# Kernel optimization log

Hardware: AMD Instinct MI355X
Metric: run time of the kernel (lower is better)

Reference implementation:

```python
import jax, jax.numpy as jnp
import numpy as np
import math

T, B, C, F, H, LF, GF = 1024, 8, 512, 64, 8, 64, 64


def setup_inputs() -> dict:
    key = jax.random.key(0)
    ks = jax.random.split(key, 24)
    s = 0.02  # weight init scale for stability through the recurrence
    rn = lambda k, shp, sc=1.0: jax.random.normal(k, shp, jnp.float32) * sc
    inp = {
        "x": rn(ks[0], (B, T, C)),
        "ln_g": jnp.ones((C,), jnp.float32),
        "ln_b": jnp.zeros((C,), jnp.float32),
        "tl_initial": rn(ks[1], (C,)),
        "tl_premix": jax.random.uniform(ks[2], (C,), jnp.float32),
        "tl_w1": rn(ks[3], (C, LF), s), "tl_b1": jnp.zeros((LF,), jnp.float32),
        "tl_w2": rn(ks[4], (LF, C), s), "tl_b2": jnp.zeros((C,), jnp.float32),
        "bias": jnp.zeros((C,), jnp.float32),
        "gating_res": jax.random.uniform(ks[5], (C,), jnp.float32),
        "g_w1": rn(ks[6], (C, GF), s), "g_b1": jnp.zeros((GF,), jnp.float32),
        "g_w2": rn(ks[7], (GF, C), s), "g_b2": jnp.zeros((C,), jnp.float32),
        "dn_initial": rn(ks[8], (H, F, F)),
        "A_w": rn(ks[9], (H, C, F), s), "A_b": rn(ks[10], (H, F), s),
        "B_w": jnp.zeros((H, C, F), jnp.float32), "B_b": rn(ks[11], (H, F), s),
        "C_w": rn(ks[12], (H, C, F), s), "C_b": rn(ks[13], (H, F), s),
        "D_w": rn(ks[14], (H, C, F), s), "D_b": rn(ks[15], (H, F), s),
        "I_w": rn(ks[16], (H, C, F), s), "I_b": rn(ks[17], (H, F), s),
        "S_w": rn(ks[18], (H, C, F), s), "S_b": rn(ks[19], (H, F), s),
        "O_w": rn(ks[20], (H, F, C), s),
    }
    return inp


def _deltanet_head(y, init_state, Aw, Ab, Bw, Bb, Cw, Cb, Dw, Db, Iw, Ib, Sw, Sb, Ow):
    # y: [T, B, C]; init_state: [F, F]
    f = init_state.shape[-1]
    sf = math.sqrt(f)  # awk_safe
    a = y @ Aw + Ab   # [T,B,F]
    b = y @ Bw + Bb
    c = y @ Cw + Cb
    d = y @ Dw + Db
    i = y @ Iw + Ib
    sel = y @ Sw + Sb
    st0 = jnp.broadcast_to(init_state, (y.shape[1], f, f)).astype(y.dtype)

    def step(st, ins):
        sel_t, a_t, b_t, c_t, d_t, i_t = ins  # each [B,F]
        st = (st * jax.nn.sigmoid(i_t)[:, None, :]
              + jnp.einsum('bij,bj->bi', st, a_t)[:, :, None] * b_t[:, None, :] / sf
              + c_t[:, :, None] * d_t[:, None, :])
        out = jnp.einsum('bf,bfg->bg', sel_t, st)
        return st, out

    st, o = jax.lax.scan(step, st0, (sel, a, b, c, d, i))
    return o @ Ow, st  # [T,B,C]


def reference(x, ln_g, ln_b, tl_initial, tl_premix, tl_w1, tl_b1, tl_w2, tl_b2,
              bias, gating_res, g_w1, g_b1, g_w2, g_b2, dn_initial,
              A_w, A_b, B_w, B_b, C_w, C_b, D_w, D_b, I_w, I_b, S_w, S_b, O_w):
    xt = jnp.swapaxes(x, 0, -2)  # [T, B, C] (time_dim=-2)
    res = xt
    # LayerNorm (eps=1e-5)
    mu = jnp.mean(xt, -1, keepdims=True)
    var = jnp.mean((xt - mu) ** 2, -1, keepdims=True)
    h = (xt - mu) / jnp.sqrt(var + 1e-5) * ln_g + ln_b
    # TokenLerp (state=None -> xf[0]=initial)
    xf = jnp.concatenate([jnp.broadcast_to(tl_initial, (1,) + h.shape[1:]).astype(h.dtype), h[:-1]], axis=0)
    pm = h + (xf - h) * tl_premix
    decide = jax.nn.sigmoid(jax.nn.gelu(pm @ tl_w1 + tl_b1, approximate=False) @ tl_w2 + tl_b2)
    h = h + (xf - h) * decide
    # y starts from bias; heads are chained sequentially (y feeds next head)
    y = jnp.broadcast_to(bias, h.shape).astype(h.dtype)
    for k in range(dn_initial.shape[0]):
        y, _ = _deltanet_head(y, dn_initial[k], A_w[k], A_b[k], B_w[k], B_b[k],
                              C_w[k], C_b[k], D_w[k], D_b[k], I_w[k], I_b[k],
                              S_w[k], S_b[k], O_w[k])
    gate = jax.nn.sigmoid(jax.nn.gelu((y + h * gating_res) @ g_w1 + g_b1, approximate=False) @ g_w2 + g_b2)
    # use_residual=True path: returns res + y (no transpose back, matching source)
    return res + y * gate
```

## Files before the change

### kernel.cpp

```cpp
#include <hip/hip_runtime.h>
#include <hip/hip_bf16.h>

#define T_DIM 1024
#define B_DIM 8
#define C_DIM 512
#define F_DIM 64
#define H_DIM 8
#define CHUNK 32
#define NCHUNK 32

__device__ __forceinline__ float sigmoidf_(float v) { return 1.0f / (1.0f + __expf(-v)); }
__device__ __forceinline__ float geluf_(float v) { return 0.5f * v * (1.0f + erff(v * 0.70710678118654752f)); }
__device__ __forceinline__ float rl_(float v, int l) {
  return __uint_as_float(__builtin_amdgcn_readlane(__float_as_uint(v), l));
}

struct GemmArgs {
  const float* A; const float* W; const float* bias; float* out;
  int M, K, N;
  const float* x; const float* mu; const float* rstd;
  const float* ln_g; const float* ln_b; const float* tl_initial; const float* premix;
  const float* yv; const float* gres;
  float* h2;
  const float* Wg[6]; const float* bg[6];
};

struct AFetch {
  float4 v0, v1, v2, v3, v4;
  float s0, s1, s2, s3;
};

template<int MODE_A>
__device__ __forceinline__ AFetch a_fetch(const GemmArgs& g, int r, int c) {
  AFetch f; f.s0 = f.s1 = f.s2 = f.s3 = 0.f;
  if (MODE_A == 0) {
    f.v0 = *(const float4*)&g.A[r * g.K + c];
  } else if (MODE_A == 1) {
    const int b = r & 7, t = r >> 3;
    f.v0 = *(const float4*)&g.x[(b * T_DIM + t) * C_DIM + c];
    f.s0 = g.mu[r]; f.s1 = g.rstd[r];
    if (t > 0) {
      f.v1 = *(const float4*)&g.x[(b * T_DIM + t - 1) * C_DIM + c];
      f.s2 = g.mu[r - 8]; f.s3 = g.rstd[r - 8];
    } else {
      f.v1 = *(const float4*)&g.tl_initial[c];
    }
    f.v2 = *(const float4*)&g.ln_g[c];
    f.v3 = *(const float4*)&g.ln_b[c];
    f.v4 = *(const float4*)&g.premix[c];
  } else {
    f.v0 = *(const float4*)&g.yv[(r >> 3) * C_DIM + c];
    f.v1 = *(const float4*)&g.h2[r * C_DIM + c];
    f.v2 = *(const float4*)&g.gres[c];
  }
  return f;
}

template<int MODE_A>
__device__ __forceinline__ float4 a_combine(const AFetch& f, int r) {
  if (MODE_A == 0) return f.v0;
  float4 o;
  float* op = (float*)&o;
  const float* xa = (const float*)&f.v0;
  const float* xb = (const float*)&f.v1;
  const float* lg = (const float*)&f.v2;
  const float* lb = (const float*)&f.v3;
  const float* pm = (const float*)&f.v4;
  if (MODE_A == 1) {
    const int t = r >> 3;
    #pragma unroll
    for (int q = 0; q < 4; ++q) {
      float h  = (xa[q] - f.s0) * f.s1 * lg[q] + lb[q];
      float xf = (t == 0) ? xb[q] : (xb[q] - f.s2) * f.s3 * lg[q] + lb[q];
      op[q] = h + (xf - h) * pm[q];
    }
    return o;
  }
  #pragma unroll
  for (int q = 0; q < 4; ++q)
    op[q] = xa[q] + xb[q] * lg[q];
  return o;
}

template<int MODE_B>
__device__ __forceinline__ float4 w_fetch(const GemmArgs& g, int kk, int n0, int tc) {
  if (MODE_B == 1)
    return *(const float4*)&g.Wg[blockIdx.y][kk * 64 + (tc << 2)];
  return *(const float4*)&g.W[kk * g.N + n0 + (tc << 2)];
}

template<int MODE_A, int MODE_B, int EPI>
__global__ __launch_bounds__(256) void gemm_kernel(GemmArgs g) {
  __shared__ float AsT[16][68];
  __shared__ float Bs[16][64];
  const int m0 = blockIdx.x * 64, n0 = blockIdx.y * 64;
  const int tid = threadIdx.x;
  const int tr = tid >> 4, tc = tid & 15;
  const int ai = tid >> 2, aj = (tid & 3) << 2;
  const float scg = (MODE_B == 1 && blockIdx.y == 1) ? 0.125f : 1.0f;
  float acc[4][4] = {};
  AFetch fa = a_fetch<MODE_A>(g, m0 + ai, aj);
  float4 wv = w_fetch<MODE_B>(g, tr, n0, tc);
  for (int k0 = 0; k0 < g.K; k0 += 16) {
    if (k0) __syncthreads();
    const float4 av = a_combine<MODE_A>(fa, m0 + ai);
    AsT[aj + 0][ai] = av.x;
    AsT[aj + 1][ai] = av.y;
    AsT[aj + 2][ai] = av.z;
    AsT[aj + 3][ai] = av.w;
    *(float4*)&Bs[tr][tc << 2] =
        make_float4(wv.x * scg, wv.y * scg, wv.z * scg, wv.w * scg);
    if (k0 + 16 < g.K) {
      fa = a_fetch<MODE_A>(g, m0 + ai, k0 + 16 + aj);
      wv = w_fetch<MODE_B>(g, k0 + 16 + tr, n0, tc);
    }
    __syncthreads();
    #pragma unroll
    for (int kk = 0; kk < 16; ++kk) {
      const float4 a4 = *(const float4*)&AsT[kk][tr << 2];
      const float4 b4 = *(const float4*)&Bs[kk][tc << 2];
      const float avr[4] = {a4.x, a4.y, a4.z, a4.w};
      const float bvr[4] = {b4.x, b4.y, b4.z, b4.w};
      #pragma unroll
      for (int r_ = 0; r_ < 4; ++r_)
        #pragma unroll
        for (int c_ = 0; c_ < 4; ++c_)
          acc[r_][c_] = fmaf(avr[r_], bvr[c_], acc[r_][c_]);
    }
  }
  #pragma unroll
  for (int r_ = 0; r_ < 4; ++r_) {
    const int rr = m0 + (tr << 2) + r_;
    #pragma unroll
    for (int c_ = 0; c_ < 4; ++c_) {
      const int lc = (tc << 2) + c_;
      const int cc = n0 + lc;
      float v = acc[r_][c_];
      if (MODE_B == 1) v += g.bg[blockIdx.y][lc] * scg;
      else if (g.bias) v += g.bias[cc];
      if (EPI == 0) {
        g.out[rr * g.N + cc] = v;
      } else if (EPI == 1) {
        g.out[rr * g.N + cc] = geluf_(v);
      } else if (EPI == 2) {
        float d = sigmoidf_(v);
        const int b = rr & 7, t = rr >> 3;
        float xv = g.x[(b * T_DIM + t) * C_DIM + cc];
        float h = (xv - g.mu[rr]) * g.rstd[rr] * g.ln_g[cc] + g.ln_b[cc];
        float xf;
        if (t == 0) xf = g.tl_initial[cc];
        else {
          float xp = g.x[(b * T_DIM + t - 1) * C_DIM + cc];
          xf = (xp - g.mu[rr - 8]) * g.rstd[rr - 8] * g.ln_g[cc] + g.ln_b[cc];
        }
        g.h2[rr * C_DIM + cc] = h + (xf - h) * d;
      } else {
        float gate = sigmoidf_(v);
        const int b = rr & 7, t = rr >> 3;
        float res = g.x[(b * T_DIM + t) * C_DIM + cc];
        g.out[rr * C_DIM + cc] = res + g.yv[t * C_DIM + cc] * gate;
      }
    }
  }
}

__global__ __launch_bounds__(256) void ln_stats_kernel(const float* __restrict__ x,
                                                       float* __restrict__ mu,
                                                       float* __restrict__ rstd,
                                                       const float* __restrict__ bias,
                                                       float* __restrict__ y) {
  const int gid = blockIdx.x * 256 + threadIdx.x;
  y[gid] = bias[gid & (C_DIM - 1)];
  const int row = blockIdx.x * 4 + (threadIdx.x >> 6);
  const int lane = threadIdx.x & 63;
  const int b = row & 7, t = row >> 3;
  const float* xr = x + (b * T_DIM + t) * C_DIM;
  float4 v0 = *(const float4*)&xr[lane * 8];
  float4 v1 = *(const float4*)&xr[lane * 8 + 4];
  float s  = v0.x + v0.y + v0.z + v0.w + v1.x + v1.y + v1.z + v1.w;
  float s2 = v0.x*v0.x + v0.y*v0.y + v0.z*v0.z + v0.w*v0.w
           + v1.x*v1.x + v1.y*v1.y + v1.z*v1.z + v1.w*v1.w;
  #pragma unroll
  for (int m = 1; m < 64; m <<= 1) { s += __shfl_xor(s, m); s2 += __shfl_xor(s2, m); }
  if (lane == 0) {
    float mean = s * (1.0f / 512.0f);
    float var = s2 * (1.0f / 512.0f) - mean * mean;
    mu[row] = mean;
    rstd[row] = rsqrtf(var + 1e-5f);
  }
}


__global__ __launch_bounds__(256) void scan_phaseA(const float* __restrict__ PRJ,
                                                   float* __restrict__ chPT,
                                                   float* __restrict__ chS) {
  const int j = blockIdx.x;
  const int tid = threadIdx.x;
  const int ri = tid >> 4, ci = tid & 15;
  float Pm[4][4], Sm[4][4];
  #pragma unroll
  for (int r = 0; r < 4; ++r)
    #pragma unroll
    for (int c = 0; c < 4; ++c) {
      Pm[r][c] = (ri * 4 + r == ci * 4 + c) ? 1.0f : 0.0f;
      Sm[r][c] = 0.0f;
    }
  const float* base = PRJ + j * CHUNK * 384;
  float4 pa = *(const float4*)&base[      ci * 4];
  float4 pb = *(const float4*)&base[ 64 + ci * 4];
  float4 pc = *(const float4*)&base[128 + ri * 4];
  float4 pd = *(const float4*)&base[192 + ci * 4];
  float4 pi = *(const float4*)&base[256 + ci * 4];
  for (int s = 0; s < CHUNK; ++s) {
    float4 na = pa, nb = pb, nc2 = pc, nd = pd, ni = pi;
    if (s + 1 < CHUNK) {
      const float* b2 = base + (s + 1) * 384;
      na  = *(const float4*)&b2[      ci * 4];
      nb  = *(const float4*)&b2[ 64 + ci * 4];
      nc2 = *(const float4*)&b2[128 + ri * 4];
      nd  = *(const float4*)&b2[192 + ci * 4];
      ni  = *(const float4*)&b2[256 + ci * 4];
    }
    const float sg[4] = {sigmoidf_(pi.x), sigmoidf_(pi.y), sigmoidf_(pi.z), sigmoidf_(pi.w)};
    const float aa[4] = {pa.x, pa.y, pa.z, pa.w};
    const float bb2[4] = {pb.x, pb.y, pb.z, pb.w};
    const float cv[4] = {pc.x, pc.y, pc.z, pc.w};
    const float dd[4] = {pd.x, pd.y, pd.z, pd.w};
    float rp[4], rs[4];
    #pragma unroll
    for (int r = 0; r < 4; ++r) {
      rp[r] = Pm[r][0]*aa[0] + Pm[r][1]*aa[1] + Pm[r][2]*aa[2] + Pm[r][3]*aa[3];
      rs[r] = Sm[r][0]*aa[0] + Sm[r][1]*aa[1] + Sm[r][2]*aa[2] + Sm[r][3]*aa[3];
    }
    #pragma unroll
    for (int m = 1; m <= 8; m <<= 1) {
      #pragma unroll
      for (int r = 0; r < 4; ++r) {
        rp[r] += __shfl_xor(rp[r], m);
        rs[r] += __shfl_xor(rs[r], m);
      }
    }
    #pragma unroll
    for (int r = 0; r < 4; ++r)
      #pragma unroll
      for (int c = 0; c < 4; ++c) {
        Pm[r][c] = Pm[r][c] * sg[c] + rp[r] * bb2[c];
        Sm[r][c] = Sm[r][c] * sg[c] + rs[r] * bb2[c] + cv[r] * dd[c];
      }
    pa = na; pb = nb; pc = nc2; pd = nd; pi = ni;
  }
  float* cpT = chPT + j * 4096;
  float* cs  = chS + j * 4096;
  #pragma unroll
  for (int c = 0; c < 4; ++c)
    *(float4*)&cpT[(ci*4+c)*64 + ri*4] =
        make_float4(Pm[0][c], Pm[1][c], Pm[2][c], Pm[3][c]);
  #pragma unroll
  for (int r = 0; r < 4; ++r)
    *(float4*)&cs[(ri*4+r)*64 + ci*4] = make_float4(Sm[r][0], Sm[r][1], Sm[r][2], Sm[r][3]);
}

__device__ __forceinline__ float cstep(const float4 (&P)[16], float sv, float rv) {
  float p0 = 0.f, p1 = 0.f, p2 = 0.f, p3 = 0.f;
  #pragma unroll
  for (int q = 0; q < 16; ++q) {
    p0 = fmaf(rl_(rv, q * 4 + 0), P[q].x, p0);
    p1 = fmaf(rl_(rv, q * 4 + 1), P[q].y, p1);
    p2 = fmaf(rl_(rv, q * 4 + 2), P[q].z, p2);
    p3 = fmaf(rl_(rv, q * 4 + 3), P[q].w, p3);
  }
  return sv + ((p0 + p1) + (p2 + p3));
}

__global__ __launch_bounds__(64) void scan_combine(const float* __restrict__ st0,
                                                   const float* __restrict__ chPT,
                                                   const float* __restrict__ chS,
                                                   float* __restrict__ bnd) {
  const int lane = threadIdx.x;
  const int r = blockIdx.x;
  float rv = st0[r * 64 + lane];
  const float* basePT = chPT + lane * 64;
  const float* baseS  = chS + r * 64 + lane;
  float* bndRL = bnd + r * 64 + lane;
  for (int j = 0; j < NCHUNK; ++j) {
    float4 P[16];
    const float* pp = basePT + j * 4096;
    #pragma unroll
    for (int q = 0; q < 16; ++q) P[q] = *(const float4*)&pp[q * 4];
    const float sv = baseS[j * 4096];
    bndRL[j * 4096] = rv;
    rv = cstep(P, sv, rv);
  }
}

__global__ __launch_bounds__(256) void scan_phaseC(const float* __restrict__ PRJ,
                                                   const float* __restrict__ bnd,
                                                   const float* __restrict__ Ow,
                                                   float* __restrict__ y) {
  __shared__ float olds[CHUNK][4][64];
  __shared__ float osT[64][CHUNK + 1];
  const int j = blockIdx.x;
  const int tid = threadIdx.x;
  const int ri = tid >> 4, ci = tid & 15, w = tid >> 6;
  float st[4][4];
  #pragma unroll
  for (int r = 0; r < 4; ++r) {
    const float4 v = *(const float4*)&bnd[j*4096 + (ri*4+r)*64 + ci*4];
    st[r][0] = v.x; st[r][1] = v.y; st[r][2] = v.z; st[r][3] = v.w;
  }
  const float* base = PRJ + j * CHUNK * 384;
  float4 pa = *(const float4*)&base[      ci * 4];
  float4 pb = *(const float4*)&base[ 64 + ci * 4];
  float4 pc = *(const float4*)&base[128 + ri * 4];
  float4 pd = *(const float4*)&base[192 + ci * 4];
  float4 pi = *(const float4*)&base[256 + ci * 4];
  float4 ps = *(const float4*)&base[320 + ri * 4];
  for (int s = 0; s < CHUNK; ++s) {
    float4 na = pa, nb = pb, nc2 = pc, nd = pd, ni = pi, ns = ps;
    if (s + 1 < CHUNK) {
      const float* b2 = base + (s + 1) * 384;
      na  = *(const float4*)&b2[      ci * 4];
      nb  = *(const float4*)&b2[ 64 + ci * 4];
      nc2 = *(const float4*)&b2[128 + ri * 4];
      nd  = *(const float4*)&b2[192 + ci * 4];
      ni  = *(const float4*)&b2[256 + ci * 4];
      ns  = *(const float4*)&b2[320 + ri * 4];
    }
    const float sg[4] = {sigmoidf_(pi.x), sigmoidf_(pi.y), sigmoidf_(pi.z), sigmoidf_(pi.w)};
    const float aa[4] = {pa.x, pa.y, pa.z, pa.w};
    const float bb2[4] = {pb.x, pb.y, pb.z, pb.w};
    const float cv[4] = {pc.x, pc.y, pc.z, pc.w};
    const float dd[4] = {pd.x, pd.y, pd.z, pd.w};
    const float ss[4] = {ps.x, ps.y, ps.z, ps.w};
    float rd[4];
    #pragma unroll
    for (int r = 0; r < 4; ++r)
      rd[r] = st[r][0]*aa[0] + st[r][1]*aa[1] + st[r][2]*aa[2] + st[r][3]*aa[3];
    #pragma unroll
    for (int m = 1; m <= 8; m <<= 1) {
      #pragma unroll
      for (int r = 0; r < 4; ++r) rd[r] += __shfl_xor(rd[r], m);
    }
    float po[4] = {0.f, 0.f, 0.f, 0.f};
    #pragma unroll
    for (int r = 0; r < 4; ++r)
      #pragma unroll
      for (int c = 0; c < 4; ++c) {
        const float nv = st[r][c] * sg[c] + rd[r] * bb2[c] + cv[r] * dd[c];
        st[r][c] = nv;
        po[c] = fmaf(ss[r], nv, po[c]);
      }
    #pragma unroll
    for (int c = 0; c < 4; ++c) {
      po[c] += __shfl_xor(po[c], 16);
      po[c] += __shfl_xor(po[c], 32);
    }
    if ((tid & 48) == 0)
      *(float4*)&olds[s][w][ci * 4] = make_float4(po[0], po[1], po[2], po[3]);
    pa = na; pb = nb; pc = nc2; pd = nd; pi = ni; ps = ns;
  }
  __syncthreads();
  #pragma unroll
  for (int e = 0; e < 8; ++e) {
    const int id = tid + 256 * e;
    const int f = id & 63, t = id >> 6;
    osT[f][t] = olds[t][0][f] + olds[t][1][f] + olds[t][2][f] + olds[t][3][f];
  }
  __syncthreads();
  const int c0 = tid << 1;
  float2 acc[CHUNK];
  #pragma unroll
  for (int t = 0; t < CHUNK; ++t) acc[t] = make_float2(0.f, 0.f);
  #pragma unroll 1
  for (int fo = 0; fo < 8; ++fo) {
    float2 ow[8];
    #pragma unroll
    for (int q = 0; q < 8; ++q)
      ow[q] = *(const float2*)&Ow[(fo * 8 + q) * C_DIM + c0];
    #pragma unroll
    for (int q = 0; q < 8; ++q) {
      const int f = fo * 8 + q;
      #pragma unroll
      for (int t8 = 0; t8 < 8; ++t8) {
        const float4 ov = *(const float4*)&osT[f][t8 * 4];
        acc[t8*4+0].x = fmaf(ov.x, ow[q].x, acc[t8*4+0].x);
        acc[t8*4+0].y = fmaf(ov.x, ow[q].y, acc[t8*4+0].y);
        acc[t8*4+1].x = fmaf(ov.y, ow[q].x, acc[t8*4+1].x);
        acc[t8*4+1].y = fmaf(ov.y, ow[q].y, acc[t8*4+1].y);
        acc[t8*4+2].x = fmaf(ov.z, ow[q].x, acc[t8*4+2].x);
        acc[t8*4+2].y = fmaf(ov.z, ow[q].y, acc[t8*4+2].y);
        acc[t8*4+3].x = fmaf(ov.w, ow[q].x, acc[t8*4+3].x);
        acc[t8*4+3].y = fmaf(ov.w, ow[q].y, acc[t8*4+3].y);
      }
    }
  }
  #pragma unroll
  for (int t = 0; t < CHUNK; ++t)
    *(float2*)&y[(j * CHUNK + t) * C_DIM + c0] = acc[t];
}

extern "C" void kernel_launch(void* const* d_in, const int* in_sizes, int n_in,
                              void* d_out, int out_size, void* d_ws, size_t ws_size,
                              hipStream_t stream) {
  const float* x       = (const float*)d_in[0];
  const float* ln_g    = (const float*)d_in[1];
  const float* ln_b    = (const float*)d_in[2];
  const float* tl_init = (const float*)d_in[3];
  const float* premix  = (const float*)d_in[4];
  const float* tl_w1   = (const float*)d_in[5];
  const float* tl_b1   = (const float*)d_in[6];
  const float* tl_w2   = (const float*)d_in[7];
  const float* tl_b2   = (const float*)d_in[8];
  const float* bias    = (const float*)d_in[9];
  const float* gres    = (const float*)d_in[10];
  const float* g_w1    = (const float*)d_in[11];
  const float* g_b1    = (const float*)d_in[12];
  const float* g_w2    = (const float*)d_in[13];
  const float* g_b2    = (const float*)d_in[14];
  const float* dn_init = (const float*)d_in[15];
  const float* A_w     = (const float*)d_in[16];
  const float* A_b     = (const float*)d_in[17];
  const float* B_w     = (const float*)d_in[18];
  const float* B_b     = (const float*)d_in[19];
  const float* C_w     = (const float*)d_in[20];
  const float* C_b     = (const float*)d_in[21];
  const float* D_w     = (const float*)d_in[22];
  const float* D_b     = (const float*)d_in[23];
  const float* I_w     = (const float*)d_in[24];
  const float* I_b     = (const float*)d_in[25];
  const float* S_w     = (const float*)d_in[26];
  const float* S_b     = (const float*)d_in[27];
  const float* O_w     = (const float*)d_in[28];

  float* ws      = (float*)d_ws;
  float* mu      = ws;
  float* rstd    = mu + 8192;
  float* hidden1 = rstd + 8192;
  float* y       = hidden1 + 524288;
  float* PRJ     = y + 524288;
  float* chPT    = PRJ + 393216;
  float* chS     = chPT + 131072;
  float* bnd     = chS + 131072;
  float* h2      = (float*)d_out;

  ln_stats_kernel<<<2048, 256, 0, stream>>>(x, mu, rstd, bias, y);

  GemmArgs ga = {};
  ga.x = x; ga.mu = mu; ga.rstd = rstd; ga.ln_g = ln_g; ga.ln_b = ln_b;
  ga.tl_initial = tl_init; ga.premix = premix; ga.gres = gres; ga.h2 = h2;

  {
    GemmArgs g = ga; g.W = tl_w1; g.bias = tl_b1; g.out = hidden1;
    g.M = 8192; g.K = 512; g.N = 64;
    gemm_kernel<1, 0, 1><<<dim3(128, 1), 256, 0, stream>>>(g);
  }
  {
    GemmArgs g = ga; g.A = hidden1; g.W = tl_w2; g.bias = tl_b2;
    g.M = 8192; g.K = 64; g.N = 512;
    gemm_kernel<0, 0, 2><<<dim3(128, 8), 256, 0, stream>>>(g);
  }

  for (int k = 0; k < H_DIM; ++k) {
    {
      GemmArgs g = ga; g.A = y; g.out = PRJ; g.M = 1024; g.K = 512; g.N = 384;
      const int woff = k * C_DIM * F_DIM, boff = k * F_DIM;
      g.Wg[0] = A_w + woff; g.Wg[1] = B_w + woff; g.Wg[2] = C_w + woff;
      g.Wg[3] = D_w + woff; g.Wg[4] = I_w + woff; g.Wg[5] = S_w + woff;
      g.bg[0] = A_b + boff; g.bg[1] = B_b + boff; g.bg[2] = C_b + boff;
      g.bg[3] = D_b + boff; g.bg[4] = I_b + boff; g.bg[5] = S_b + boff;
      gemm_kernel<0, 1, 0><<<dim3(16, 6), 256, 0, stream>>>(g);
    }
    scan_phaseA<<<NCHUNK, 256, 0, stream>>>(PRJ, chPT, chS);
    scan_combine<<<64, 64, 0, stream>>>(dn_init + k * 4096, chPT, chS, bnd);
    scan_phaseC<<<NCHUNK, 256, 0, stream>>>(PRJ, bnd, O_w + k * F_DIM * C_DIM, y);
  }

  {
    GemmArgs g = ga; g.yv = y; g.W = g_w1; g.bias = g_b1; g.out = hidden1;
    g.M = 8192; g.K = 512; g.N = 64;
    gemm_kernel<2, 0, 1><<<dim3(128, 1), 256, 0, stream>>>(g);
  }
  {
    GemmArgs g = ga; g.yv = y; g.A = hidden1; g.W = g_w2; g.bias = g_b2;
    g.out = (float*)d_out; g.M = 8192; g.K = 64; g.N = 512;
    gemm_kernel<0, 0, 3><<<dim3(128, 8), 256, 0, stream>>>(g);
  }
}
```

Before: 966.2 us.

## Fuse scan combine and phase C with per-chunk flag handoff

```diff
diff --git a/kernel.cpp b/kernel.cpp
--- a/kernel.cpp
+++ b/kernel.cpp
@@ -193,9 +193,11 @@
 
 __global__ __launch_bounds__(256) void scan_phaseA(const float* __restrict__ PRJ,
                                                    float* __restrict__ chPT,
-                                                   float* __restrict__ chS) {
+                                                   float* __restrict__ chS,
+                                                   int* __restrict__ flags) {
   const int j = blockIdx.x;
   const int tid = threadIdx.x;
+  if (tid == 0) flags[j] = 0;
   const int ri = tid >> 4, ci = tid & 15;
   float Pm[4][4], Sm[4][4];
   #pragma unroll
@@ -272,35 +274,40 @@
   return sv + ((p0 + p1) + (p2 + p3));
 }
 
-__global__ __launch_bounds__(64) void scan_combine(const float* __restrict__ st0,
-                                                   const float* __restrict__ chPT,
-                                                   const float* __restrict__ chS,
-                                                   float* __restrict__ bnd) {
-  const int lane = threadIdx.x;
-  const int r = blockIdx.x;
-  float rv = st0[r * 64 + lane];
-  const float* basePT = chPT + lane * 64;
-  const float* baseS  = chS + r * 64 + lane;
-  float* bndRL = bnd + r * 64 + lane;
-  for (int j = 0; j < NCHUNK; ++j) {
-    float4 P[16];
-    const float* pp = basePT + j * 4096;
-    #pragma unroll
-    for (int q = 0; q < 16; ++q) P[q] = *(const float4*)&pp[q * 4];
-    const float sv = baseS[j * 4096];
-    bndRL[j * 4096] = rv;
-    rv = cstep(P, sv, rv);
-  }
-}
-
-__global__ __launch_bounds__(256) void scan_phaseC(const float* __restrict__ PRJ,
-                                                   const float* __restrict__ bnd,
-                                                   const float* __restrict__ Ow,
-                                                   float* __restrict__ y) {
+__global__ __launch_bounds__(256) void combineC_kernel(
+    const float* __restrict__ st0, const float* __restrict__ chPT,
+    const float* __restrict__ chS, float* __restrict__ bnd,
+    const float* __restrict__ PRJ, const float* __restrict__ Ow,
+    float* __restrict__ y, int* __restrict__ flags) {
   __shared__ float olds[CHUNK][4][64];
   __shared__ float osT[64][CHUNK + 1];
-  const int j = blockIdx.x;
   const int tid = threadIdx.x;
+  if (blockIdx.x < 16) {
+    const int lane = tid & 63;
+    const int r = blockIdx.x * 4 + (tid >> 6);
+    float rv = st0[r * 64 + lane];
+    const float* basePT = chPT + lane * 64;
+    const float* baseS  = chS + r * 64 + lane;
+    float* bndRL = bnd + r * 64 + lane;
+    for (int j = 0; j < NCHUNK; ++j) {
+      float4 P[16];
+      const float* pp = basePT + j * 4096;
+      #pragma unroll
+      for (int q = 0; q < 16; ++q) P[q] = *(const float4*)&pp[q * 4];
+      const float sv = baseS[j * 4096];
+      bndRL[j * 4096] = rv;
+      __threadfence();
+      if (lane == 0) atomicAdd(&flags[j], 1);
+      rv = cstep(P, sv, rv);
+    }
+    return;
+  }
+  const int j = blockIdx.x - 16;
+  if (tid == 0) {
+    while (__hip_atomic_load(flags + j, __ATOMIC_ACQUIRE,
+                             __HIP_MEMORY_SCOPE_AGENT) < 64) {}
+  }
+  __syncthreads();
   const int ri = tid >> 4, ci = tid & 15, w = tid >> 6;
   float st[4][4];
   #pragma unroll
@@ -441,6 +448,7 @@
   float* chPT    = PRJ + 393216;
   float* chS     = chPT + 131072;
   float* bnd     = chS + 131072;
+  int*   flags   = (int*)(bnd + 131072);
   float* h2      = (float*)d_out;
 
   ln_stats_kernel<<<2048, 256, 0, stream>>>(x, mu, rstd, bias, y);
@@ -470,9 +478,9 @@
       g.bg[3] = D_b + boff; g.bg[4] = I_b + boff; g.bg[5] = S_b + boff;
       gemm_kernel<0, 1, 0><<<dim3(16, 6), 256, 0, stream>>>(g);
     }
-    scan_phaseA<<<NCHUNK, 256, 0, stream>>>(PRJ, chPT, chS);
-    scan_combine<<<64, 64, 0, stream>>>(dn_init + k * 4096, chPT, chS, bnd);
-    scan_phaseC<<<NCHUNK, 256, 0, stream>>>(PRJ, bnd, O_w + k * F_DIM * C_DIM, y);
+    scan_phaseA<<<NCHUNK, 256, 0, stream>>>(PRJ, chPT, chS, flags);
+    combineC_kernel<<<48, 256, 0, stream>>>(dn_init + k * 4096, chPT, chS, bnd,
+                                            PRJ, O_w + k * F_DIM * C_DIM, y, flags);
   }
 
   {
```

After: 2.148 ms. 122% more time.
